# Performance work log

Hardware: AMD Instinct MI355X
Metric: run time of the kernel (lower is better)

Reference implementation:

```python
import jax, jax.numpy as jnp
import numpy as np

ALPHA = 0.2  # leaky relu slope
NEG_BIG = -9000000000000000.0


def setup_inputs() -> dict:
    key = jax.random.key(0)
    k1, k2, k3, k4 = jax.random.split(key, 4)
    B, N, Fin, Fout = 8, 2048, 256, 256
    h = jax.random.normal(k1, (B, N, Fin), dtype=jnp.float32)
    adj = jax.random.randint(k2, (B, N, N), 0, 2, dtype=jnp.int32)
    # xavier_uniform with gain=1.414
    gain = 1.414
    limW = gain * np.sqrt(6.0 / (Fin + Fout))
    W = jax.random.uniform(k3, (Fin, Fout), dtype=jnp.float32, minval=-limW, maxval=limW)
    lima = gain * np.sqrt(6.0 / (2 * Fout + 1))
    a = jax.random.uniform(k4, (2 * Fout, 1), dtype=jnp.float32, minval=-lima, maxval=lima)
    return {"h": h, "adj": adj, "W": W, "a": a}


def reference(h, adj, W, a):
    # Wh: [B, N, F]
    Wh = jnp.matmul(h, W)
    Fout = W.shape[1]
    a1 = a[:Fout, 0]   # scores for source node i (repeat_interleave side)
    a2 = a[Fout:, 0]   # scores for target node j (repeat side)
    # e[b,i,j] = leakyrelu(Wh[b,i]@a1 + Wh[b,j]@a2)  -- decomposed, no O(N^2 * 2F) tensor
    s1 = jnp.einsum('bnf,f->bn', Wh, a1)  # [B, N]
    s2 = jnp.einsum('bnf,f->bn', Wh, a2)  # [B, N]
    e = jax.nn.leaky_relu(s1[:, :, None] + s2[:, None, :], negative_slope=ALPHA)
    masked = jnp.where(adj > 0, e, jnp.full_like(e, NEG_BIG))
    attention = jax.nn.softmax(masked, axis=2)  # dropout=0 (eval mode)
    h_prime = jnp.matmul(attention, Wh)  # [B, N, F]
    return jax.nn.elu(h_prime)
```

## Files before the change

### kernel.cpp

```cpp
#include <hip/hip_runtime.h>

typedef __attribute__((ext_vector_type(8))) short bhalf8;
typedef __attribute__((ext_vector_type(4))) float floatx4;

#define ALPHA_LR 0.2f

__device__ __forceinline__ unsigned short f2bf(float f) {
  union { float f; unsigned int u; } v; v.f = f;
  unsigned int r = v.u + 0x7fffu + ((v.u >> 16) & 1u);
  return (unsigned short)(r >> 16);
}
__device__ __forceinline__ float bf2f(unsigned short u) {
  union { unsigned int u; float f; } v; v.u = ((unsigned int)u) << 16;
  return v.f;
}

__global__ __launch_bounds__(256) void k0h_split(const float* __restrict__ h,
                                                 unsigned short* __restrict__ Ahi,
                                                 unsigned short* __restrict__ Alo) {
  const int idx = blockIdx.x * 256 + threadIdx.x;
  float4 x = ((const float4*)h)[idx];
  ushort4 hi, lo;
  float xs[4] = {x.x, x.y, x.z, x.w};
  unsigned short hs[4], ls[4];
#pragma unroll
  for (int q = 0; q < 4; q++) {
    hs[q] = f2bf(xs[q]);
    ls[q] = f2bf(xs[q] - bf2f(hs[q]));
  }
  hi = (ushort4){hs[0], hs[1], hs[2], hs[3]};
  lo = (ushort4){ls[0], ls[1], ls[2], ls[3]};
  ((ushort4*)Ahi)[idx] = hi;
  ((ushort4*)Alo)[idx] = lo;
}

__global__ void k0w_split(const float* __restrict__ W,
                          unsigned short* __restrict__ WThi,
                          unsigned short* __restrict__ WTlo) {
  __shared__ float s[16][17];
  const int tx = threadIdx.x, ty = threadIdx.y;
  const int n0 = blockIdx.x * 16, k0 = blockIdx.y * 16;
  s[ty][tx] = W[(k0 + ty) * 256 + n0 + tx];
  __syncthreads();
  float v = s[tx][ty];
  unsigned short hi = f2bf(v);
  unsigned short lo = f2bf(v - bf2f(hi));
  WThi[(n0 + ty) * 256 + k0 + tx] = hi;
  WTlo[(n0 + ty) * 256 + k0 + tx] = lo;
}

__global__ __launch_bounds__(512) void k1_mfma(const unsigned short* __restrict__ Ahi_g,
                                               const unsigned short* __restrict__ Alo_g,
                                               const unsigned short* __restrict__ Bhi_g,
                                               const unsigned short* __restrict__ Blo_g,
                                               const float* __restrict__ a_g,
                                               unsigned short* __restrict__ WhPack,
                                               float* __restrict__ s1,
                                               float* __restrict__ s2) {
  __shared__ unsigned short Ah[64 * 264], Al[64 * 264];
  __shared__ unsigned short Bh[256 * 40], Bl[256 * 40];
  __shared__ float s1red[64], s2red[64];
  const int t = threadIdx.x;
  const long r0 = (long)blockIdx.x * 64;

  if (t < 64) { s1red[t] = 0.f; s2red[t] = 0.f; }

  {
    const int4* srcH = (const int4*)(Ahi_g + r0 * 256);
    const int4* srcL = (const int4*)(Alo_g + r0 * 256);
#pragma unroll
    for (int q = 0; q < 4; q++) {
      int cid = q * 512 + t;
      int row = cid >> 5, col8 = cid & 31;
      int4 vh = srcH[cid];
      int4 vl = srcL[cid];
      *(int4*)&Ah[row * 264 + col8 * 8] = vh;
      *(int4*)&Al[row * 264 + col8 * 8] = vl;
    }
  }

  const int wave = t >> 6, lane = t & 63;
  const int wm = wave >> 2, wn = wave & 3;
  const int lhi = lane >> 4, llo = lane & 15;

  floatx4 acc[2][4];
#pragma unroll
  for (int mt = 0; mt < 2; mt++)
#pragma unroll
    for (int nt = 0; nt < 4; nt++) acc[mt][nt] = (floatx4){0.f, 0.f, 0.f, 0.f};

  for (int ks = 0; ks < 8; ks++) {
    const int k0 = ks * 32;
    int4 vh[2], vl[2];
#pragma unroll
    for (int q = 0; q < 2; q++) {
      int cid = q * 512 + t;
      int n = cid >> 2, c = cid & 3;
      vh[q] = *(const int4*)(Bhi_g + n * 256 + k0 + c * 8);
      vl[q] = *(const int4*)(Blo_g + n * 256 + k0 + c * 8);
    }
    __syncthreads();
#pragma unroll
    for (int q = 0; q < 2; q++) {
      int cid = q * 512 + t;
      int n = cid >> 2, c = cid & 3;
      *(int4*)&Bh[n * 40 + c * 8] = vh[q];
      *(int4*)&Bl[n * 40 + c * 8] = vl[q];
    }
    __syncthreads();

    bhalf8 ah[2], al[2], bh[4], bl[4];
#pragma unroll
    for (int mt = 0; mt < 2; mt++) {
      int ro = (wm * 32 + mt * 16 + llo) * 264 + k0 + lhi * 8;
      ah[mt] = *(const bhalf8*)&Ah[ro];
      al[mt] = *(const bhalf8*)&Al[ro];
    }
#pragma unroll
    for (int nt = 0; nt < 4; nt++) {
      int ro = (wn * 64 + nt * 16 + llo) * 40 + lhi * 8;
      bh[nt] = *(const bhalf8*)&Bh[ro];
      bl[nt] = *(const bhalf8*)&Bl[ro];
    }
#pragma unroll
    for (int mt = 0; mt < 2; mt++)
#pragma unroll
      for (int nt = 0; nt < 4; nt++) {
        acc[mt][nt] = __builtin_amdgcn_mfma_f32_16x16x32_bf16(ah[mt], bh[nt], acc[mt][nt], 0, 0, 0);
        acc[mt][nt] = __builtin_amdgcn_mfma_f32_16x16x32_bf16(ah[mt], bl[nt], acc[mt][nt], 0, 0, 0);
        acc[mt][nt] = __builtin_amdgcn_mfma_f32_16x16x32_bf16(al[mt], bh[nt], acc[mt][nt], 0, 0, 0);
      }
  }

  float a1v[4], a2v[4];
#pragma unroll
  for (int nt = 0; nt < 4; nt++) {
    int f = wn * 64 + nt * 16 + llo;
    a1v[nt] = a_g[f];
    a2v[nt] = a_g[256 + f];
  }

  const int b = (int)(r0 >> 11);
  const int jt_base = (int)((r0 & 2047) >> 5);

#pragma unroll
  for (int mt = 0; mt < 2; mt++) {
    float p1[4], p2[4];
#pragma unroll
    for (int reg = 0; reg < 4; reg++) {
      p1[reg] = acc[mt][0][reg] * a1v[0] + acc[mt][1][reg] * a1v[1] +
                acc[mt][2][reg] * a1v[2] + acc[mt][3][reg] * a1v[3];
      p2[reg] = acc[mt][0][reg] * a2v[0] + acc[mt][1][reg] * a2v[1] +
                acc[mt][2][reg] * a2v[2] + acc[mt][3][reg] * a2v[3];
    }
#pragma unroll
    for (int off = 1; off < 16; off <<= 1) {
#pragma unroll
      for (int reg = 0; reg < 4; reg++) {
        p1[reg] += __shfl_xor(p1[reg], off);
        p2[reg] += __shfl_xor(p2[reg], off);
      }
    }
    if (llo == 0) {
#pragma unroll
      for (int reg = 0; reg < 4; reg++) {
        int il = wm * 32 + mt * 16 + lhi * 4 + reg;
        atomicAdd(&s1red[il], p1[reg]);
        atomicAdd(&s2red[il], p2[reg]);
      }
    }
#pragma unroll
    for (int nt = 0; nt < 4; nt++) {
      int f = wn * 64 + nt * 16 + llo;
      int jt = jt_base + wm;
      ushort4 pk = (ushort4){f2bf(acc[mt][nt][0]), f2bf(acc[mt][nt][1]),
                             f2bf(acc[mt][nt][2]), f2bf(acc[mt][nt][3])};
      *(ushort4*)&WhPack[((long)((b * 64 + jt) * 256 + f)) * 32 + mt * 16 + lhi * 4] = pk;
    }
  }

  __syncthreads();
  if (t < 64) {
    s1[r0 + t] = s1red[t];
    s2[r0 + t] = s2red[t];
  }
}

__global__ __launch_bounds__(256) void k2_stats(const int* __restrict__ adj,
                                                const float* __restrict__ s1,
                                                const float* __restrict__ s2,
                                                float* __restrict__ Mv,
                                                float* __restrict__ linv,
                                                unsigned int* __restrict__ packed) {
  const int t = threadIdx.x;
  const long r = blockIdx.x;
  const int b = (int)(r >> 11);
  __shared__ float red[4];
  __shared__ int redi[4];
  __shared__ unsigned char bytes[256];

  const int4* arow = (const int4*)(adj + r * 2048);
  int4 a0 = arow[t * 2], a1 = arow[t * 2 + 1];
  unsigned int m8 = (unsigned)(a0.x > 0) | ((unsigned)(a0.y > 0) << 1) |
                    ((unsigned)(a0.z > 0) << 2) | ((unsigned)(a0.w > 0) << 3) |
                    ((unsigned)(a1.x > 0) << 4) | ((unsigned)(a1.y > 0) << 5) |
                    ((unsigned)(a1.z > 0) << 6) | ((unsigned)(a1.w > 0) << 7);

  int cnt = __popc(m8);
  for (int o = 32; o; o >>= 1) cnt += __shfl_xor(cnt, o);
  if ((t & 63) == 0) redi[t >> 6] = cnt;
  __syncthreads();
  int total = redi[0] + redi[1] + redi[2] + redi[3];
  if (total == 0) m8 = 0xFFu;

  const float4* s2p = (const float4*)(s2 + (long)b * 2048);
  float4 v0 = s2p[t * 2], v1 = s2p[t * 2 + 1];
  float sv[8] = {v0.x, v0.y, v0.z, v0.w, v1.x, v1.y, v1.z, v1.w};

  float mx = -INFINITY;
#pragma unroll
  for (int q = 0; q < 8; q++)
    if ((m8 >> q) & 1) mx = fmaxf(mx, sv[q]);
  for (int o = 32; o; o >>= 1) mx = fmaxf(mx, __shfl_xor(mx, o));
  if ((t & 63) == 0) red[t >> 6] = mx;
  __syncthreads();
  mx = fmaxf(fmaxf(red[0], red[1]), fmaxf(red[2], red[3]));

  const float s1i = s1[r];
  const float xm = s1i + mx;
  const float M = xm > 0.f ? xm : ALPHA_LR * xm;

  float lsum = 0.f;
#pragma unroll
  for (int q = 0; q < 8; q++) {
    if ((m8 >> q) & 1) {
      float x = s1i + sv[q];
      float le = x > 0.f ? x : ALPHA_LR * x;
      lsum += __expf(le - M);
    }
  }
  for (int o = 32; o; o >>= 1) lsum += __shfl_xor(lsum, o);
  __syncthreads();
  if ((t & 63) == 0) red[t >> 6] = lsum;
  __syncthreads();
  lsum = red[0] + red[1] + red[2] + red[3];

  if (t == 0) { Mv[r] = M; linv[r] = 1.f / lsum; }

  bytes[t] = (unsigned char)m8;
  __syncthreads();
  if (t < 64) {
    unsigned int w = (unsigned)bytes[t * 4] | ((unsigned)bytes[t * 4 + 1] << 8) |
                     ((unsigned)bytes[t * 4 + 2] << 16) | ((unsigned)bytes[t * 4 + 3] << 24);
    packed[r * 64 + t] = w;
  }
}

__global__ __launch_bounds__(512) void k3_attn(const unsigned short* __restrict__ WhPack,
                                               const unsigned int* __restrict__ packed,
                                               const float* __restrict__ s1,
                                               const float* __restrict__ s2,
                                               const float* __restrict__ Mv,
                                               const float* __restrict__ linv,
                                               float* __restrict__ out) {
  const int t = threadIdx.x;
  const int it = blockIdx.x;
  const int b = blockIdx.y;
  const int i0 = it * 32;

  __shared__ float s2all[2048];
  __shared__ unsigned int bits[2048];
  __shared__ float s1v[32], Mvv[32], lvv[32];
  __shared__ unsigned short WhT[256 * 40];
  __shared__ unsigned short P[32 * 40];

  {
    const float4* src = (const float4*)(s2 + (long)b * 2048);
    ((float4*)s2all)[t] = src[t];
  }
  {
    const int4* src = (const int4*)(packed + ((long)b * 2048 + i0) * 64);
    ((int4*)bits)[t] = src[t];
  }
  if (t < 32) {
    long r = (long)b * 2048 + i0 + t;
    s1v[t] = s1[r]; Mvv[t] = Mv[r]; lvv[t] = linv[r];
  }
  __syncthreads();

  const int wave = t >> 6, lane = t & 63;
  const int wm = wave >> 2, wn = wave & 3;
  const int lhi = lane >> 4, llo = lane & 15;
  const int i_p = t >> 4;
  const int jl0 = (t & 15) * 2;

  floatx4 acc[4];
#pragma unroll
  for (int nt = 0; nt < 4; nt++) acc[nt] = (floatx4){0.f, 0.f, 0.f, 0.f};

  for (int jt = 0; jt < 64; jt++) {
    const int4* wsrc = (const int4*)(WhPack + ((long)(b * 64 + jt) * 256) * 32);
#pragma unroll
    for (int rep = 0; rep < 2; rep++) {
      int cid = rep * 512 + t;
      int f = cid >> 2, c = cid & 3;
      int4 v = wsrc[cid];
      *(int4*)&WhT[f * 40 + c * 8] = v;
    }
    {
      unsigned int w = bits[i_p * 64 + jt];
      float s1i = s1v[i_p], Mi = Mvv[i_p];
      unsigned short pb[2];
#pragma unroll
      for (int q = 0; q < 2; q++) {
        int jl = jl0 + q;
        float x = s1i + s2all[jt * 32 + jl];
        float le = x > 0.f ? x : ALPHA_LR * x;
        float pu = ((w >> jl) & 1u) ? __expf(le - Mi) : 0.f;
        pb[q] = f2bf(pu);
      }
      *(unsigned int*)&P[i_p * 40 + jl0] = (unsigned)pb[0] | ((unsigned)pb[1] << 16);
    }
    __syncthreads();

    bhalf8 af = *(const bhalf8*)&P[(wm * 16 + llo) * 40 + lhi * 8];
    bhalf8 bf[4];
#pragma unroll
    for (int nt = 0; nt < 4; nt++)
      bf[nt] = *(const bhalf8*)&WhT[(wn * 64 + nt * 16 + llo) * 40 + lhi * 8];
#pragma unroll
    for (int nt = 0; nt < 4; nt++)
      acc[nt] = __builtin_amdgcn_mfma_f32_16x16x32_bf16(af, bf[nt], acc[nt], 0, 0, 0);
    __syncthreads();
  }

#pragma unroll
  for (int nt = 0; nt < 4; nt++) {
#pragma unroll
    for (int reg = 0; reg < 4; reg++) {
      int il = wm * 16 + lhi * 4 + reg;
      int f = wn * 64 + nt * 16 + llo;
      float v = acc[nt][reg] * lvv[il];
      v = v > 0.f ? v : expm1f(v);
      out[((long)(b * 2048 + i0 + il)) * 256 + f] = v;
    }
  }
}

extern "C" void kernel_launch(void* const* d_in, const int* in_sizes, int n_in,
                              void* d_out, int out_size, void* d_ws, size_t ws_size,
                              hipStream_t stream) {
  const float* h = (const float*)d_in[0];
  const int* adj = (const int*)d_in[1];
  const float* W = (const float*)d_in[2];
  const float* a = (const float*)d_in[3];
  float* out = (float*)d_out;

  char* ws = (char*)d_ws;
  unsigned short* WhPack = (unsigned short*)ws;
  unsigned short* Ahi = (unsigned short*)(ws + 8388608);
  unsigned short* Alo = (unsigned short*)(ws + 16777216);
  unsigned int* packed = (unsigned int*)(ws + 16777216);
  unsigned short* WThi = (unsigned short*)(ws + 25165824);
  unsigned short* WTlo = (unsigned short*)(ws + 25296896);
  float* s1 = (float*)(ws + 25427968);
  float* s2 = (float*)(ws + 25493504);
  float* Mv = (float*)(ws + 25559040);
  float* linv = (float*)(ws + 25624576);

  hipLaunchKernelGGL(k0h_split, dim3(4096), dim3(256), 0, stream, h, Ahi, Alo);
  hipLaunchKernelGGL(k0w_split, dim3(16, 16), dim3(16, 16), 0, stream, W, WThi, WTlo);
  hipLaunchKernelGGL(k1_mfma, dim3(256), dim3(512), 0, stream, Ahi, Alo, WThi, WTlo, a,
                     WhPack, s1, s2);
  hipLaunchKernelGGL(k2_stats, dim3(16384), dim3(256), 0, stream, adj, s1, s2, Mv, linv, packed);
  hipLaunchKernelGGL(k3_attn, dim3(64, 8), dim3(512), 0, stream, WhPack, packed, s1, s2, Mv, linv, out);
}
```

Baseline: 301.1 us.

## Fuse h bf16 split into GEMM and double-buffer tiles via direct global-to-LDS loads

Removes the separate h split kernel by converting h to hi/lo bf16 inside the Wh GEMM. W is repacked into per-k-slice contiguous tiles so B tiles, and the Wh tiles in the attention kernel, can be fetched with global_load_lds straight into double-buffered shared memory, prefetching the next tile while the current one feeds MFMA. Each loop iteration now has one barrier instead of two. The change also adds launch-bounds occupancy hints and uses fmaxf for leaky ReLU. It relies on correct completion ordering of the async LDS loads before the barrier, and the padding-free LDS layout may cause bank conflicts.

```diff
diff --git a/kernel.cpp b/kernel.cpp
--- a/kernel.cpp
+++ b/kernel.cpp
@@ -14,24 +14,10 @@
   union { unsigned int u; float f; } v; v.u = ((unsigned int)u) << 16;
   return v.f;
 }
-
-__global__ __launch_bounds__(256) void k0h_split(const float* __restrict__ h,
-                                                 unsigned short* __restrict__ Ahi,
-                                                 unsigned short* __restrict__ Alo) {
-  const int idx = blockIdx.x * 256 + threadIdx.x;
-  float4 x = ((const float4*)h)[idx];
-  ushort4 hi, lo;
-  float xs[4] = {x.x, x.y, x.z, x.w};
-  unsigned short hs[4], ls[4];
-#pragma unroll
-  for (int q = 0; q < 4; q++) {
-    hs[q] = f2bf(xs[q]);
-    ls[q] = f2bf(xs[q] - bf2f(hs[q]));
-  }
-  hi = (ushort4){hs[0], hs[1], hs[2], hs[3]};
-  lo = (ushort4){ls[0], ls[1], ls[2], ls[3]};
-  ((ushort4*)Ahi)[idx] = hi;
-  ((ushort4*)Alo)[idx] = lo;
+__device__ __forceinline__ void gld16(const void* g, void* l) {
+  __builtin_amdgcn_global_load_lds((const __attribute__((address_space(1))) unsigned int*)g,
+                                   (__attribute__((address_space(3))) unsigned int*)l,
+                                   16, 0, 0);
 }
 
 __global__ void k0w_split(const float* __restrict__ W,
@@ -43,43 +29,54 @@
   s[ty][tx] = W[(k0 + ty) * 256 + n0 + tx];
   __syncthreads();
   float v = s[tx][ty];
+  const int k = k0 + tx, n = n0 + ty;
   unsigned short hi = f2bf(v);
   unsigned short lo = f2bf(v - bf2f(hi));
-  WThi[(n0 + ty) * 256 + k0 + tx] = hi;
-  WTlo[(n0 + ty) * 256 + k0 + tx] = lo;
-}
-
-__global__ __launch_bounds__(512) void k1_mfma(const unsigned short* __restrict__ Ahi_g,
-                                               const unsigned short* __restrict__ Alo_g,
-                                               const unsigned short* __restrict__ Bhi_g,
-                                               const unsigned short* __restrict__ Blo_g,
-                                               const float* __restrict__ a_g,
-                                               unsigned short* __restrict__ WhPack,
-                                               float* __restrict__ s1,
-                                               float* __restrict__ s2) {
+  const int idx = (k >> 5) * 8192 + n * 32 + (k & 31);
+  WThi[idx] = hi;
+  WTlo[idx] = lo;
+}
+
+__global__ __launch_bounds__(512, 2) void k1_mfma(const float* __restrict__ h,
+                                                  const unsigned short* __restrict__ Bhi_g,
+                                                  const unsigned short* __restrict__ Blo_g,
+                                                  const float* __restrict__ a_g,
+                                                  unsigned short* __restrict__ WhPack,
+                                                  float* __restrict__ s1,
+                                                  float* __restrict__ s2) {
   __shared__ unsigned short Ah[64 * 264], Al[64 * 264];
-  __shared__ unsigned short Bh[256 * 40], Bl[256 * 40];
+  __shared__ unsigned short Bh[2][8192], Bl[2][8192];
   __shared__ float s1red[64], s2red[64];
   const int t = threadIdx.x;
   const long r0 = (long)blockIdx.x * 64;
+  const int wave = t >> 6, lane = t & 63;
 
   if (t < 64) { s1red[t] = 0.f; s2red[t] = 0.f; }
 
-  {
-    const int4* srcH = (const int4*)(Ahi_g + r0 * 256);
-    const int4* srcL = (const int4*)(Alo_g + r0 * 256);
-#pragma unroll
-    for (int q = 0; q < 4; q++) {
-      int cid = q * 512 + t;
-      int row = cid >> 5, col8 = cid & 31;
-      int4 vh = srcH[cid];
-      int4 vl = srcL[cid];
-      *(int4*)&Ah[row * 264 + col8 * 8] = vh;
-      *(int4*)&Al[row * 264 + col8 * 8] = vl;
-    }
-  }
-
-  const int wave = t >> 6, lane = t & 63;
+#pragma unroll
+  for (int rep = 0; rep < 2; rep++) {
+    const int off = wave * 1024 + rep * 512;
+    gld16(Bhi_g + off + lane * 8, &Bh[0][off]);
+    gld16(Blo_g + off + lane * 8, &Bl[0][off]);
+  }
+
+#pragma unroll
+  for (int q = 0; q < 8; q++) {
+    int idx = q * 512 + t;
+    int row = idx >> 6, c4 = idx & 63;
+    float4 x = *(const float4*)(h + (r0 + row) * 256 + c4 * 4);
+    float xs[4] = {x.x, x.y, x.z, x.w};
+    unsigned short hs[4], ls[4];
+#pragma unroll
+    for (int qq = 0; qq < 4; qq++) {
+      hs[qq] = f2bf(xs[qq]);
+      ls[qq] = f2bf(xs[qq] - bf2f(hs[qq]));
+    }
+    *(ushort4*)&Ah[row * 264 + c4 * 4] = (ushort4){hs[0], hs[1], hs[2], hs[3]};
+    *(ushort4*)&Al[row * 264 + c4 * 4] = (ushort4){ls[0], ls[1], ls[2], ls[3]};
+  }
+  __syncthreads();
+
   const int wm = wave >> 2, wn = wave & 3;
   const int lhi = lane >> 4, llo = lane & 15;
 
@@ -90,25 +87,15 @@
     for (int nt = 0; nt < 4; nt++) acc[mt][nt] = (floatx4){0.f, 0.f, 0.f, 0.f};
 
   for (int ks = 0; ks < 8; ks++) {
+    const int cur = ks & 1, nxt = cur ^ 1, ksn = (ks + 1) & 7;
+#pragma unroll
+    for (int rep = 0; rep < 2; rep++) {
+      const int off = wave * 1024 + rep * 512;
+      gld16(Bhi_g + ksn * 8192 + off + lane * 8, &Bh[nxt][off]);
+      gld16(Blo_g + ksn * 8192 + off + lane * 8, &Bl[nxt][off]);
+    }
+
     const int k0 = ks * 32;
-    int4 vh[2], vl[2];
-#pragma unroll
-    for (int q = 0; q < 2; q++) {
-      int cid = q * 512 + t;
-      int n = cid >> 2, c = cid & 3;
-      vh[q] = *(const int4*)(Bhi_g + n * 256 + k0 + c * 8);
-      vl[q] = *(const int4*)(Blo_g + n * 256 + k0 + c * 8);
-    }
-    __syncthreads();
-#pragma unroll
-    for (int q = 0; q < 2; q++) {
-      int cid = q * 512 + t;
-      int n = cid >> 2, c = cid & 3;
-      *(int4*)&Bh[n * 40 + c * 8] = vh[q];
-      *(int4*)&Bl[n * 40 + c * 8] = vl[q];
-    }
-    __syncthreads();
-
     bhalf8 ah[2], al[2], bh[4], bl[4];
 #pragma unroll
     for (int mt = 0; mt < 2; mt++) {
@@ -118,9 +105,9 @@
     }
 #pragma unroll
     for (int nt = 0; nt < 4; nt++) {
-      int ro = (wn * 64 + nt * 16 + llo) * 40 + lhi * 8;
-      bh[nt] = *(const bhalf8*)&Bh[ro];
-      bl[nt] = *(const bhalf8*)&Bl[ro];
+      int ro = (wn * 64 + nt * 16 + llo) * 32 + lhi * 8;
+      bh[nt] = *(const bhalf8*)&Bh[cur][ro];
+      bl[nt] = *(const bhalf8*)&Bl[cur][ro];
     }
 #pragma unroll
     for (int mt = 0; mt < 2; mt++)
@@ -130,6 +117,7 @@
         acc[mt][nt] = __builtin_amdgcn_mfma_f32_16x16x32_bf16(ah[mt], bl[nt], acc[mt][nt], 0, 0, 0);
         acc[mt][nt] = __builtin_amdgcn_mfma_f32_16x16x32_bf16(al[mt], bh[nt], acc[mt][nt], 0, 0, 0);
       }
+    __syncthreads();
   }
 
   float a1v[4], a2v[4];
@@ -228,14 +216,14 @@
 
   const float s1i = s1[r];
   const float xm = s1i + mx;
-  const float M = xm > 0.f ? xm : ALPHA_LR * xm;
+  const float M = fmaxf(xm, ALPHA_LR * xm);
 
   float lsum = 0.f;
 #pragma unroll
   for (int q = 0; q < 8; q++) {
     if ((m8 >> q) & 1) {
       float x = s1i + sv[q];
-      float le = x > 0.f ? x : ALPHA_LR * x;
+      float le = fmaxf(x, ALPHA_LR * x);
       lsum += __expf(le - M);
     }
   }
@@ -256,13 +244,13 @@
   }
 }
 
-__global__ __launch_bounds__(512) void k3_attn(const unsigned short* __restrict__ WhPack,
-                                               const unsigned int* __restrict__ packed,
-                                               const float* __restrict__ s1,
-                                               const float* __restrict__ s2,
-                                               const float* __restrict__ Mv,
-                                               const float* __restrict__ linv,
-                                               float* __restrict__ out) {
+__global__ __launch_bounds__(512, 4) void k3_attn(const unsigned short* __restrict__ WhPack,
+                                                  const unsigned int* __restrict__ packed,
+                                                  const float* __restrict__ s1,
+                                                  const float* __restrict__ s2,
+                                                  const float* __restrict__ Mv,
+                                                  const float* __restrict__ linv,
+                                                  float* __restrict__ out) {
   const int t = threadIdx.x;
   const int it = blockIdx.x;
   const int b = blockIdx.y;
@@ -271,8 +259,8 @@
   __shared__ float s2all[2048];
   __shared__ unsigned int bits[2048];
   __shared__ float s1v[32], Mvv[32], lvv[32];
-  __shared__ unsigned short WhT[256 * 40];
-  __shared__ unsigned short P[32 * 40];
+  __shared__ unsigned short WhT[2][8192];
+  __shared__ unsigned short P[2][1280];
 
   {
     const float4* src = (const float4*)(s2 + (long)b * 2048);
@@ -294,40 +282,60 @@
   const int i_p = t >> 4;
   const int jl0 = (t & 15) * 2;
 
+  const unsigned short* tbase = WhPack + ((long)b * 64) * 8192;
+
+#pragma unroll
+  for (int rep = 0; rep < 2; rep++) {
+    const int off = wave * 1024 + rep * 512;
+    gld16(tbase + off + lane * 8, &WhT[0][off]);
+  }
+  {
+    unsigned int w = bits[i_p * 64 + 0];
+    float s1i = s1v[i_p], Mi = Mvv[i_p];
+    unsigned short pb[2];
+#pragma unroll
+    for (int q = 0; q < 2; q++) {
+      int jl = jl0 + q;
+      float x = s1i + s2all[jl];
+      float le = fmaxf(x, ALPHA_LR * x);
+      float pu = ((w >> jl) & 1u) ? __expf(le - Mi) : 0.f;
+      pb[q] = f2bf(pu);
+    }
+    *(unsigned int*)&P[0][i_p * 40 + jl0] = (unsigned)pb[0] | ((unsigned)pb[1] << 16);
+  }
+  __syncthreads();
+
   floatx4 acc[4];
 #pragma unroll
   for (int nt = 0; nt < 4; nt++) acc[nt] = (floatx4){0.f, 0.f, 0.f, 0.f};
 
   for (int jt = 0; jt < 64; jt++) {
-    const int4* wsrc = (const int4*)(WhPack + ((long)(b * 64 + jt) * 256) * 32);
+    const int cur = jt & 1, nxt = cur ^ 1, jtn = (jt + 1) & 63;
+
 #pragma unroll
     for (int rep = 0; rep < 2; rep++) {
-      int cid = rep * 512 + t;
-      int f = cid >> 2, c = cid & 3;
-      int4 v = wsrc[cid];
-      *(int4*)&WhT[f * 40 + c * 8] = v;
+      const int off = wave * 1024 + rep * 512;
+      gld16(tbase + jtn * 8192 + off + lane * 8, &WhT[nxt][off]);
     }
     {
-      unsigned int w = bits[i_p * 64 + jt];
+      unsigned int w = bits[i_p * 64 + jtn];
       float s1i = s1v[i_p], Mi = Mvv[i_p];
       unsigned short pb[2];
 #pragma unroll
       for (int q = 0; q < 2; q++) {
         int jl = jl0 + q;
-        float x = s1i + s2all[jt * 32 + jl];
-        float le = x > 0.f ? x : ALPHA_LR * x;
+        float x = s1i + s2all[jtn * 32 + jl];
+        float le = fmaxf(x, ALPHA_LR * x);
         float pu = ((w >> jl) & 1u) ? __expf(le - Mi) : 0.f;
         pb[q] = f2bf(pu);
       }
-      *(unsigned int*)&P[i_p * 40 + jl0] = (unsigned)pb[0] | ((unsigned)pb[1] << 16);
-    }
-    __syncthreads();
-
-    bhalf8 af = *(const bhalf8*)&P[(wm * 16 + llo) * 40 + lhi * 8];
+      *(unsigned int*)&P[nxt][i_p * 40 + jl0] = (unsigned)pb[0] | ((unsigned)pb[1] << 16);
+    }
+    bhalf8 af = *(const bhalf8*)&P[cur][(wm * 16 + llo) * 40 + lhi * 8];
     bhalf8 bf[4];
 #pragma unroll
     for (int nt = 0; nt < 4; nt++)
-      bf[nt] = *(const bhalf8*)&WhT[(wn * 64 + nt * 16 + llo) * 40 + lhi * 8];
+      bf[nt] = *(const bhalf8*)&WhT[cur][(wn * 64 + nt * 16 + llo) * 32 + lhi * 8];
 #pragma unroll
     for (int nt = 0; nt < 4; nt++)
       acc[nt] = __builtin_amdgcn_mfma_f32_16x16x32_bf16(af, bf[nt], acc[nt], 0, 0, 0);
@@ -358,19 +366,16 @@
 
   char* ws = (char*)d_ws;
   unsigned short* WhPack = (unsigned short*)ws;
-  unsigned short* Ahi = (unsigned short*)(ws + 8388608);
-  unsigned short* Alo = (unsigned short*)(ws + 16777216);
-  unsigned int* packed = (unsigned int*)(ws + 16777216);
-  unsigned short* WThi = (unsigned short*)(ws + 25165824);
-  unsigned short* WTlo = (unsigned short*)(ws + 25296896);
-  float* s1 = (float*)(ws + 25427968);
-  float* s2 = (float*)(ws + 25493504);
-  float* Mv = (float*)(ws + 25559040);
-  float* linv = (float*)(ws + 25624576);
-
-  hipLaunchKernelGGL(k0h_split, dim3(4096), dim3(256), 0, stream, h, Ahi, Alo);
+  unsigned int* packed = (unsigned int*)(ws + 8388608);
+  unsigned short* WThi = (unsigned short*)(ws + 12582912);
+  unsigned short* WTlo = (unsigned short*)(ws + 12713984);
+  float* s1 = (float*)(ws + 12845056);
+  float* s2 = (float*)(ws + 12910592);
+  float* Mv = (float*)(ws + 12976128);
+  float* linv = (float*)(ws + 13041664);
+
   hipLaunchKernelGGL(k0w_split, dim3(16, 16), dim3(16, 16), 0, stream, W, WThi, WTlo);
-  hipLaunchKernelGGL(k1_mfma, dim3(256), dim3(512), 0, stream, Ahi, Alo, WThi, WTlo, a,
+  hipLaunchKernelGGL(k1_mfma, dim3(256), dim3(512), 0, stream, h, WThi, WTlo, a,
                      WhPack, s1, s2);
   hipLaunchKernelGGL(k2_stats, dim3(16384), dim3(256), 0, stream, adj, s1, s2, Mv, linv, packed);
   hipLaunchKernelGGL(k3_attn, dim3(64, 8), dim3(512), 0, stream, WhPack, packed, s1, s2, Mv, linv, out);
```

Measured after the change: 265.4 us. -11.9%, faster.
